# Kernel optimization log

Measured on AMD Instinct MI355X. Metric: run time of the kernel, lower is better.

## Reference

```python
import jax, jax.numpy as jnp
import numpy as np

EPS = 1e-5  # BatchNorm1d default eps
E = 64      # embedding_dim
H = 64      # h_dim


def _mlp(x, W1, b1, gamma, beta, W2, b2):
    # Linear -> BatchNorm1d (training-mode batch stats) -> ReLU -> Linear
    h = x @ W1.T + b1
    mu = h.mean(axis=0)
    var = h.var(axis=0)  # biased variance, as BatchNorm normalization uses
    h = jax.nn.relu((h - mu) * jax.lax.rsqrt(var + EPS) * gamma + beta)
    return h @ W2.T + b2


def _lstm_step(h, c, x, Wih, Whh, bih, bhh):
    # PyTorch LSTM gate order: i, f, g, o
    gates = x @ Wih.T + bih + h @ Whh.T + bhh
    i, f, g, o = jnp.split(gates, 4, axis=-1)
    c = jax.nn.sigmoid(f) * c + jax.nn.sigmoid(i) * jnp.tanh(g)
    h = jax.nn.sigmoid(o) * jnp.tanh(c)
    return h, c


def setup_inputs() -> dict:
    key = jax.random.key(0)
    ks = jax.random.split(key, 16)
    OBS_LEN, BATCH = 8, 131072
    f32 = jnp.float32
    inp = {
        "obs_traj": jax.random.uniform(ks[0], (OBS_LEN, BATCH, 2), dtype=f32) * 100.0,
        # spatial_embedding MLP: [2, 16, 64]
        "se_W1": jax.random.normal(ks[1], (16, 2), f32) * 0.5,
        "se_b1": jnp.zeros((16,), f32),
        "se_gamma": jnp.ones((16,), f32),
        "se_beta": jnp.zeros((16,), f32),
        "se_W2": jax.random.normal(ks[2], (E, 16), f32) * 0.2,
        "se_b2": jnp.zeros((E,), f32),
        # hidden2pos MLP: [64, 16, 2]
        "hp_W1": jax.random.normal(ks[3], (16, H), f32) * 0.1,
        "hp_b1": jnp.zeros((16,), f32),
        "hp_gamma": jnp.ones((16,), f32),
        "hp_beta": jnp.zeros((16,), f32),
        "hp_W2": jax.random.normal(ks[4], (2, 16), f32) * 0.2,
        "hp_b2": jnp.zeros((2,), f32),
        # LSTM(64, 64, num_layers=1)
        "Wih": jax.random.normal(ks[5], (4 * H, E), f32) * 0.1,
        "Whh": jax.random.normal(ks[6], (4 * H, H), f32) * 0.1,
        "bih": jnp.zeros((4 * H,), f32),
        "bhh": jnp.zeros((4 * H,), f32),
        "x_max": 100,
        "y_max": 100,
        "pred_len": 12,
    }
    return inp


def reference(obs_traj, se_W1, se_b1, se_gamma, se_beta, se_W2, se_b2,
              hp_W1, hp_b1, hp_gamma, hp_beta, hp_W2, hp_b2,
              Wih, Whh, bih, bhh, x_max, y_max, pred_len):
    T, B, _ = obs_traj.shape
    xy_max = jnp.asarray([x_max, y_max], dtype=obs_traj.dtype)
    obs = obs_traj / xy_max  # (T, B, 2)

    # embed observed trajectory: (T*B, 2) -> (T, B, E)
    emb = _mlp(obs.reshape(-1, 2), se_W1, se_b1, se_gamma, se_beta, se_W2, se_b2)
    emb = emb.reshape(T, B, E)

    h0 = jnp.zeros((B, H), obs.dtype)
    c0 = jnp.zeros((B, H), obs.dtype)

    def enc(carry, x):
        h, c = carry
        h, c = _lstm_step(h, c, x, Wih, Whh, bih, bhh)
        return (h, c), None

    (h, c), _ = jax.lax.scan(enc, (h0, c0), emb)

    def dec(carry, _):
        h, c, last_pos = carry
        pos_rel = _mlp(h, hp_W1, hp_b1, hp_gamma, hp_beta, hp_W2, hp_b2)  # (B, 2)
        # relative_to_abs over a single step == pos_rel + last_pos
        last_pos = jax.nn.sigmoid(pos_rel + last_pos)
        x = _mlp(last_pos, se_W1, se_b1, se_gamma, se_beta, se_W2, se_b2)  # (B, E)
        h, c = _lstm_step(h, c, x, Wih, Whh, bih, bhh)
        return (h, c, last_pos), last_pos

    _, pred = jax.lax.scan(dec, (h, c, obs[-1]), None, length=pred_len)
    return pred * xy_max  # (pred_len, B, 2)
```

## Files before the change

kernel.cpp:

```cpp
#include <hip/hip_runtime.h>
#include <math.h>


#define TT 8
#define PLEN 12
#define ROWS 64
#define NBUCK 16
#define XSTR 112

typedef unsigned short u16;
typedef short short8 __attribute__((ext_vector_type(8)));
typedef float f4 __attribute__((ext_vector_type(4)));
union U8 { u16 u[8]; short8 v; };

#define ST_ENCM 0
#define ST_HP(d)  (128 + (d)*512)
#define ST_MOM(d) (128 + PLEN*512 + (d)*128)
#define ST_TOTAL  (128 + PLEN*512 + PLEN*128)

struct KP {
  const float *obs;
  const float *seW1,*seb1,*seg,*sebeta,*seW2,*seb2;
  const float *hpW1,*hpb1,*hpg,*hpbeta,*hpW2,*hpb2;
  const float *Wih,*Whh,*bih,*bhh;
  const int *xmax,*ymax;
  float *c,*lastpos,*avalg,*M,*gbias,*gbc;
  u16 *Xg1,*Xg2,*Xg3,*W1G,*W2G,*W3G,*H1G,*H2G,*H3G;
  double *stats;
  float *out;
  int B;
};

__device__ __forceinline__ float finv(float d){
  float r = __builtin_amdgcn_rcpf(d);
  return r*(2.f - d*r);
}
__device__ __forceinline__ float sigf(float x){
  float z = fminf(fmaxf(-x, -80.f), 80.f);
  return finv(1.f + __expf(z));
}
__device__ __forceinline__ float tanhf_(float x){
  float z = fminf(fmaxf(2.f*x, -80.f), 80.f);
  return 1.f - 2.f*finv(__expf(z) + 1.f);
}
__device__ __forceinline__ u16 f2bf(float x){
  union{float f; unsigned u;} v; v.f = x;
  unsigned r = v.u + 0x7FFFu + ((v.u >> 16) & 1u);
  return (u16)(r >> 16);
}
__device__ __forceinline__ float bf2f(u16 b){
  union{unsigned u; float f;} v; v.u = ((unsigned)b) << 16; return v.f;
}
__device__ __forceinline__ void split3(float x, u16& a, u16& b, u16& c){
  a = f2bf(x);
  float r1 = x - bf2f(a);
  b = f2bf(r1);
  float r2 = r1 - bf2f(b);
  c = f2bf(r2);
}

#define MF6(A1c,A2c,A3c,b1,b2,b3,accv) \
  accv = __builtin_amdgcn_mfma_f32_16x16x32_bf16(A1c, b1, accv, 0,0,0); \
  accv = __builtin_amdgcn_mfma_f32_16x16x32_bf16(A1c, b2, accv, 0,0,0); \
  accv = __builtin_amdgcn_mfma_f32_16x16x32_bf16(A2c, b1, accv, 0,0,0); \
  accv = __builtin_amdgcn_mfma_f32_16x16x32_bf16(A2c, b2, accv, 0,0,0); \
  accv = __builtin_amdgcn_mfma_f32_16x16x32_bf16(A1c, b3, accv, 0,0,0); \
  accv = __builtin_amdgcn_mfma_f32_16x16x32_bf16(A3c, b1, accv, 0,0,0);

__device__ __forceinline__ void fold_se_mom(const KP& P, const double* stb, double N,
                                            float* sef, int tid){
  if (tid < 16){
    double Sx=0, Sy=0, Sxx=0, Syy=0, Sxy=0;
    for (int b = 0; b < NBUCK; ++b){
      const double* m = stb + b*8;
      Sx += m[0]; Sy += m[1]; Sxx += m[2]; Syy += m[3]; Sxy += m[4];
    }
    double a = (double)P.seW1[2*tid], bb = (double)P.seW1[2*tid+1], cb = (double)P.seb1[tid];
    double S1 = a*Sx + bb*Sy + N*cb;
    double S2 = a*a*Sxx + bb*bb*Syy + 2.0*a*bb*Sxy + 2.0*a*cb*Sx + 2.0*bb*cb*Sy + N*cb*cb;
    double mu = S1/N, var = S2/N - mu*mu;
    float sc = rsqrtf((float)var + 1e-5f) * P.seg[tid];
    float sh = P.sebeta[tid] - (float)mu*sc;
    sef[tid]      = P.seW1[2*tid]*sc;
    sef[16 + tid] = P.seW1[2*tid+1]*sc;
    sef[32 + tid] = P.seb1[tid]*sc + sh;
  }
}

__device__ __forceinline__ void do_epilogue(f4 (&acc)[2][4], float (&cr)[2][4],
                                            u16* X1, u16* X2, u16* X3,
                                            bool first, int lane, int wid){
  const int c = lane & 15, q = lane >> 4;
  #pragma unroll
  for (int ci = 0; ci < 2; ++ci){
    const int j = (2*wid + ci)*4 + q;
    #pragma unroll
    for (int rt = 0; rt < 4; ++rt){
      const int r = rt*16 + c;
      float iv = acc[ci][rt].x, fv = acc[ci][rt].y;
      float gv = acc[ci][rt].z, ov = acc[ci][rt].w;
      float cp = first ? 0.f : cr[ci][rt];
      float cn = sigf(fv)*cp + sigf(iv)*tanhf_(gv);
      cr[ci][rt] = cn;
      float hn = sigf(ov)*tanhf_(cn);
      u16 a, b, cc2;
      split3(hn, a, b, cc2);
      X1[r*XSTR + j] = a; X2[r*XSTR + j] = b; X3[r*XSTR + j] = cc2;
    }
  }
}

__device__ __forceinline__ void tail_xg_aval(const KP& P, long row0,
                                             const u16* X1, const u16* X2, const u16* X3,
                                             double* redd, double* st,
                                             int tid, int lane, int wid, int blk){
  {
    int r = tid >> 3, ch = tid & 7;
    *(short8*)&P.Xg1[(row0 + r)*64 + ch*8] = *(const short8*)&X1[r*XSTR + ch*8];
    *(short8*)&P.Xg2[(row0 + r)*64 + ch*8] = *(const short8*)&X2[r*XSTR + ch*8];
    *(short8*)&P.Xg3[(row0 + r)*64 + ch*8] = *(const short8*)&X3[r*XSTR + ch*8];
  }
  if (wid < 4){
    const int c = lane & 15, q = lane >> 4, rt = wid;
    f4 av = *(const f4*)&P.hpb1[q*4];
    #pragma unroll
    for (int kc = 0; kc < 2; ++kc){
      const int aoff = (lane & 15)*64 + kc*32 + q*8;
      short8 HA1 = *(const short8*)&P.H1G[aoff];
      short8 HA2 = *(const short8*)&P.H2G[aoff];
      short8 HA3 = *(const short8*)&P.H3G[aoff];
      const int boff = (rt*16 + c)*XSTR + kc*32 + q*8;
      short8 b1 = *(const short8*)&X1[boff];
      short8 b2 = *(const short8*)&X2[boff];
      short8 b3 = *(const short8*)&X3[boff];
      MF6(HA1, HA2, HA3, b1, b2, b3, av);
    }
    #pragma unroll
    for (int i = 0; i < 4; ++i)
      P.avalg[(long)(q*4 + i)*P.B + row0 + rt*16 + c] = av[i];
    #pragma unroll
    for (int i = 0; i < 4; ++i){
      double s = (double)av[i];
      double s2 = s*s;
      #pragma unroll
      for (int off = 8; off; off >>= 1){
        s  += __shfl_down(s,  off, 16);
        s2 += __shfl_down(s2, off, 16);
      }
      if (c == 0){
        redd[wid*32 + q*4 + i]      = s;
        redd[wid*32 + 16 + q*4 + i] = s2;
      }
    }
  }
  __syncthreads();
  if (tid < 32){
    double s = redd[tid] + redd[32 + tid] + redd[64 + tid] + redd[96 + tid];
    atomicAdd(&st[(blk & (NBUCK-1))*32 + tid], s);
  }
}

__global__ __launch_bounds__(256) void k_prep(KP P){
  const int g = threadIdx.x;
  const float* __restrict__ wr = P.Wih + g*64;
  double gb = (double)P.bih[g] + (double)P.bhh[g];
  for (int e = 0; e < 64; ++e) gb += (double)wr[e]*(double)P.seb2[e];
  P.gbias[g] = (float)gb;
  for (int q = 0; q < 16; ++q){
    double m = 0.0;
    for (int e = 0; e < 64; ++e) m += (double)wr[e]*(double)P.seW2[e*16+q];
    P.M[g*16+q] = (float)m;
  }
}

__global__ __launch_bounds__(256) void k_prep2(KP P){
  const int cidx = threadIdx.x;
  const int gate = cidx & 3, j = cidx >> 2;
  P.gbc[cidx] = P.gbias[gate*64 + j];
  for (int k = 0; k < 96; ++k){
    float w = 0.f;
    if (k < 64)      w = P.Whh[(gate*64 + j)*64 + k];
    else if (k < 80) w = P.M[(gate*64 + j)*16 + (k - 64)];
    u16 a, b, c;
    split3(w, a, b, c);
    P.W1G[cidx*96 + k] = a;
    P.W2G[cidx*96 + k] = b;
    P.W3G[cidx*96 + k] = c;
  }
  if (cidx < 16){
    for (int k = 0; k < 64; ++k){
      u16 a, b, c;
      split3(P.hpW1[cidx*64 + k], a, b, c);
      P.H1G[cidx*64 + k] = a;
      P.H2G[cidx*64 + k] = b;
      P.H3G[cidx*64 + k] = c;
    }
  }
}

__global__ __launch_bounds__(512) void k_stats_mom(KP P){
  __shared__ double redd[5*9];
  const int tid = threadIdx.x, lane = tid & 63, wid = tid >> 6;
  const int row = blockIdx.x*512 + tid;
  const int B = P.B;
  const float xm = (float)P.xmax[0], ym = (float)P.ymax[0];
  double sx=0, sy=0, sxx=0, syy=0, sxy=0;
  #pragma unroll 1
  for (int t = 0; t < TT; ++t){
    float2 o = ((const float2*)P.obs)[(long)t*B + row];
    float x = o.x/xm, y = o.y/ym;
    sx += (double)x; sy += (double)y;
    sxx += (double)x*(double)x; syy += (double)y*(double)y;
    sxy += (double)x*(double)y;
  }
  #pragma unroll
  for (int off = 32; off; off >>= 1){
    sx  += __shfl_down(sx,  off, 64);
    sy  += __shfl_down(sy,  off, 64);
    sxx += __shfl_down(sxx, off, 64);
    syy += __shfl_down(syy, off, 64);
    sxy += __shfl_down(sxy, off, 64);
  }
  if (lane == 0){
    redd[0*9+wid]=sx; redd[1*9+wid]=sy; redd[2*9+wid]=sxx;
    redd[3*9+wid]=syy; redd[4*9+wid]=sxy;
  }
  __syncthreads();
  if (tid < 5){
    double s = 0.0;
    for (int w = 0; w < 8; ++w) s += redd[tid*9 + w];
    atomicAdd(&P.stats[ST_ENCM + (blockIdx.x & (NBUCK-1))*8 + tid], s);
  }
}

__global__ __launch_bounds__(512) void k_enc(KP P){
  __shared__ __align__(16) u16 X1[ROWS*XSTR];
  __shared__ __align__(16) u16 X2[ROWS*XSTR];
  __shared__ __align__(16) u16 X3[ROWS*XSTR];
  __shared__ float sef[48];
  __shared__ double redd[128];
  const int tid = threadIdx.x, lane = tid & 63, wid = tid >> 6;
  const int B = P.B;
  const long row0 = (long)blockIdx.x * ROWS;
  const float xm = (float)P.xmax[0], ym = (float)P.ymax[0];

  for (int m = tid; m < 3584; m += 512){
    ((unsigned*)X1)[m] = 0u; ((unsigned*)X2)[m] = 0u; ((unsigned*)X3)[m] = 0u;
  }
  fold_se_mom(P, P.stats + ST_ENCM, 8.0*(double)B, sef, tid);
  __syncthreads();

  if (tid < ROWS){
    float2 o = ((const float2*)P.obs)[row0 + tid];
    float p0 = o.x/xm, p1 = o.y/ym;
    #pragma unroll
    for (int q = 0; q < 16; ++q){
      float tv = sef[q]*p0 + sef[16+q]*p1 + sef[32+q];
      tv = tv > 0.f ? tv : 0.f;
      u16 a, b, c;
      split3(tv, a, b, c);
      X1[tid*XSTR + 64 + q] = a; X2[tid*XSTR + 64 + q] = b; X3[tid*XSTR + 64 + q] = c;
    }
  }
  __syncthreads();

  const int c = lane & 15, q = lane >> 4;
  float cr[2][4];
  f4 acc[2][4];

  #pragma unroll 1
  for (int t = 0; t < TT; ++t){
    #pragma unroll
    for (int ci = 0; ci < 2; ++ci){
      f4 bias = *(const f4*)&P.gbc[(2*wid + ci)*16 + q*4];
      #pragma unroll
      for (int rt = 0; rt < 4; ++rt) acc[ci][rt] = bias;
    }
    #pragma unroll
    for (int rt = 0; rt < 4; ++rt){
      #pragma unroll
      for (int kc = 0; kc < 3; ++kc){
        const int boff = (rt*16 + c)*XSTR + kc*32 + q*8;
        short8 b1 = *(const short8*)&X1[boff];
        short8 b2 = *(const short8*)&X2[boff];
        short8 b3 = *(const short8*)&X3[boff];
        #pragma unroll
        for (int ci = 0; ci < 2; ++ci){
          const int aoff = ((2*wid + ci)*16 + c)*96 + kc*32 + q*8;
          short8 A1 = *(const short8*)&P.W1G[aoff];
          short8 A2 = *(const short8*)&P.W2G[aoff];
          short8 A3 = *(const short8*)&P.W3G[aoff];
          MF6(A1, A2, A3, b1, b2, b3, acc[ci][rt]);
        }
      }
    }
    __syncthreads();
    do_epilogue(acc, cr, X1, X2, X3, t == 0, lane, wid);
    if (t < TT-1 && tid < ROWS){
      float2 o = ((const float2*)P.obs)[(long)(t+1)*B + row0 + tid];
      float p0 = o.x/xm, p1 = o.y/ym;
      #pragma unroll
      for (int qq = 0; qq < 16; ++qq){
        float tv = sef[qq]*p0 + sef[16+qq]*p1 + sef[32+qq];
        tv = tv > 0.f ? tv : 0.f;
        u16 a, b, cc;
        split3(tv, a, b, cc);
        X1[tid*XSTR + 64 + qq] = a; X2[tid*XSTR + 64 + qq] = b; X3[tid*XSTR + 64 + qq] = cc;
      }
    }
    __syncthreads();
  }

  #pragma unroll
  for (int ci = 0; ci < 2; ++ci){
    const int j = (2*wid + ci)*4 + q;
    #pragma unroll
    for (int rt = 0; rt < 4; ++rt)
      P.c[(long)j*B + row0 + rt*16 + c] = cr[ci][rt];
  }
  tail_xg_aval(P, row0, X1, X2, X3, redd, P.stats + ST_HP(0), tid, lane, wid, blockIdx.x);
}

template<bool FIRSTD>
__global__ __launch_bounds__(256) void k_dec_pos(KP P, int d){
  __shared__ float hpf[32];
  __shared__ double redd[5*5];
  const int tid = threadIdx.x, lane = tid & 63, wid = tid >> 6;
  const int B = P.B;
  const int row = blockIdx.x*256 + tid;
  if (tid < 16){
    const double* st = P.stats + ST_HP(d);
    double s = 0.0, s2 = 0.0;
    for (int b = 0; b < NBUCK; ++b){ s += st[b*32 + tid]; s2 += st[b*32 + 16 + tid]; }
    double invN = 1.0/(double)B;
    double mu = s*invN, var = s2*invN - mu*mu;
    float sc = rsqrtf((float)var + 1e-5f) * P.hpg[tid];
    hpf[tid] = sc;
    hpf[16+tid] = P.hpbeta[tid] - (float)mu*sc;
  }
  __syncthreads();

  float r0v = P.hpb2[0], r1v = P.hpb2[1];
  #pragma unroll
  for (int qq = 0; qq < 16; ++qq){
    float a = P.avalg[(long)qq*B + row];
    a = a*hpf[qq] + hpf[16+qq];
    a = a > 0.f ? a : 0.f;
    r0v += a*P.hpW2[qq]; r1v += a*P.hpW2[16+qq];
  }
  const float xm = (float)P.xmax[0], ym = (float)P.ymax[0];
  float l0, l1;
  if constexpr (FIRSTD){
    float2 o = ((const float2*)P.obs)[(long)(TT-1)*B + row];
    l0 = o.x/xm; l1 = o.y/ym;
  } else {
    float2 lp = ((const float2*)P.lastpos)[row];
    l0 = lp.x; l1 = lp.y;
  }
  l0 = sigf(r0v + l0);
  l1 = sigf(r1v + l1);
  ((float2*)P.lastpos)[row] = make_float2(l0, l1);
  ((float2*)P.out)[(long)d*B + row] = make_float2(l0*xm, l1*ym);

  double a0=l0, a1=l1, a2=(double)l0*(double)l0, a3=(double)l1*(double)l1, a4=(double)l0*(double)l1;
  #pragma unroll
  for (int off = 32; off; off >>= 1){
    a0 += __shfl_down(a0, off, 64); a1 += __shfl_down(a1, off, 64);
    a2 += __shfl_down(a2, off, 64); a3 += __shfl_down(a3, off, 64);
    a4 += __shfl_down(a4, off, 64);
  }
  if (lane == 0){
    redd[0*5+wid]=a0; redd[1*5+wid]=a1; redd[2*5+wid]=a2;
    redd[3*5+wid]=a3; redd[4*5+wid]=a4;
  }
  __syncthreads();
  if (tid < 5){
    double s = 0.0;
    for (int w = 0; w < 4; ++w) s += redd[tid*5 + w];
    atomicAdd(&P.stats[ST_MOM(d) + (blockIdx.x & (NBUCK-1))*8 + tid], s);
  }
}

template<int DUMMY>
__global__ __launch_bounds__(512) void k_dec_lstm(KP P, int d){
  __shared__ __align__(16) u16 X1[ROWS*XSTR];
  __shared__ __align__(16) u16 X2[ROWS*XSTR];
  __shared__ __align__(16) u16 X3[ROWS*XSTR];
  __shared__ float sef[48];
  __shared__ double redd[128];
  const int tid = threadIdx.x, lane = tid & 63, wid = tid >> 6;
  const int B = P.B;
  const long row0 = (long)blockIdx.x * ROWS;
  const int c = lane & 15, q = lane >> 4;

  fold_se_mom(P, P.stats + ST_MOM(d), (double)B, sef, tid);
  __syncthreads();

  short8 vb1[4], vb2[4], vb3[4];
  {
    const short8 z = {0,0,0,0,0,0,0,0};
    #pragma unroll
    for (int rt = 0; rt < 4; ++rt){ vb1[rt] = z; vb2[rt] = z; vb3[rt] = z; }
    if (q < 2){
      #pragma unroll
      for (int rt = 0; rt < 4; ++rt){
        float2 lp = ((const float2*)P.lastpos)[row0 + rt*16 + c];
        U8 u1, u2, u3;
        #pragma unroll
        for (int j = 0; j < 8; ++j){
          const int ch = q*8 + j;
          float tv = sef[ch]*lp.x + sef[16+ch]*lp.y + sef[32+ch];
          tv = tv > 0.f ? tv : 0.f;
          split3(tv, u1.u[j], u2.u[j], u3.u[j]);
        }
        vb1[rt] = u1.v; vb2[rt] = u2.v; vb3[rt] = u3.v;
      }
    }
  }
  float cr[2][4];
  #pragma unroll
  for (int ci = 0; ci < 2; ++ci){
    const int j = (2*wid + ci)*4 + q;
    #pragma unroll
    for (int rt = 0; rt < 4; ++rt)
      cr[ci][rt] = P.c[(long)j*B + row0 + rt*16 + c];
  }

  f4 acc[2][4];
  #pragma unroll
  for (int ci = 0; ci < 2; ++ci){
    f4 bias = *(const f4*)&P.gbc[(2*wid + ci)*16 + q*4];
    #pragma unroll
    for (int rt = 0; rt < 4; ++rt) acc[ci][rt] = bias;
  }
  #pragma unroll
  for (int rt = 0; rt < 4; ++rt){
    const long gb = (row0 + rt*16 + c)*64;
    #pragma unroll
    for (int kc = 0; kc < 2; ++kc){
      short8 b1 = *(const short8*)&P.Xg1[gb + kc*32 + q*8];
      short8 b2 = *(const short8*)&P.Xg2[gb + kc*32 + q*8];
      short8 b3 = *(const short8*)&P.Xg3[gb + kc*32 + q*8];
      #pragma unroll
      for (int ci = 0; ci < 2; ++ci){
        const int aoff = ((2*wid + ci)*16 + c)*96 + kc*32 + q*8;
        short8 A1 = *(const short8*)&P.W1G[aoff];
        short8 A2 = *(const short8*)&P.W2G[aoff];
        short8 A3 = *(const short8*)&P.W3G[aoff];
        MF6(A1, A2, A3, b1, b2, b3, acc[ci][rt]);
      }
    }
    #pragma unroll
    for (int ci = 0; ci < 2; ++ci){
      const int aoff = ((2*wid + ci)*16 + c)*96 + 2*32 + q*8;
      short8 A1 = *(const short8*)&P.W1G[aoff];
      short8 A2 = *(const short8*)&P.W2G[aoff];
      short8 A3 = *(const short8*)&P.W3G[aoff];
      MF6(A1, A2, A3, vb1[rt], vb2[rt], vb3[rt], acc[ci][rt]);
    }
  }

  do_epilogue(acc, cr, X1, X2, X3, false, lane, wid);
  #pragma unroll
  for (int ci = 0; ci < 2; ++ci){
    const int j = (2*wid + ci)*4 + q;
    #pragma unroll
    for (int rt = 0; rt < 4; ++rt)
      P.c[(long)j*B + row0 + rt*16 + c] = cr[ci][rt];
  }
  __syncthreads();
  tail_xg_aval(P, row0, X1, X2, X3, redd, P.stats + ST_HP(d+1), tid, lane, wid, blockIdx.x);
}

extern "C" void kernel_launch(void* const* d_in, const int* in_sizes, int n_in,
                              void* d_out, int out_size, void* d_ws, size_t ws_size,
                              hipStream_t stream){
  KP P;
  P.obs    = (const float*)d_in[0];
  P.seW1   = (const float*)d_in[1];
  P.seb1   = (const float*)d_in[2];
  P.seg    = (const float*)d_in[3];
  P.sebeta = (const float*)d_in[4];
  P.seW2   = (const float*)d_in[5];
  P.seb2   = (const float*)d_in[6];
  P.hpW1   = (const float*)d_in[7];
  P.hpb1   = (const float*)d_in[8];
  P.hpg    = (const float*)d_in[9];
  P.hpbeta = (const float*)d_in[10];
  P.hpW2   = (const float*)d_in[11];
  P.hpb2   = (const float*)d_in[12];
  P.Wih    = (const float*)d_in[13];
  P.Whh    = (const float*)d_in[14];
  P.bih    = (const float*)d_in[15];
  P.bhh    = (const float*)d_in[16];
  P.xmax   = (const int*)d_in[17];
  P.ymax   = (const int*)d_in[18];

  const int B = in_sizes[0] / (TT*2);
  P.B = B;
  float* ws = (float*)d_ws;
  P.Xg1     = (u16*)(ws);
  P.Xg2     = (u16*)(ws + (size_t)32*B);
  P.c       = ws + (size_t)64*B;
  P.lastpos = ws + (size_t)128*B;
  P.Xg3     = (u16*)(ws + (size_t)130*B);
  P.avalg   = ws + (size_t)162*B;
  float* tail = ws + (size_t)178*B;
  P.M     = tail;
  P.gbias = tail + 4096;
  P.gbc   = tail + 4352;
  P.W1G   = (u16*)(tail + 4608);
  P.W2G   = (u16*)(tail + 4608 + 12288);
  P.W3G   = (u16*)(tail + 4608 + 24576);
  P.H1G   = (u16*)(tail + 4608 + 36864);
  P.H2G   = (u16*)(tail + 4608 + 37376);
  P.H3G   = (u16*)(tail + 4608 + 37888);
  P.stats = (double*)(tail + 4608 + 38400);
  P.out   = (float*)d_out;

  hipMemsetAsync(P.stats, 0, ST_TOTAL*sizeof(double), stream);

  k_prep     <<<1, 256, 0, stream>>>(P);
  k_prep2    <<<1, 256, 0, stream>>>(P);
  k_stats_mom<<<B/512, 512, 0, stream>>>(P);
  k_enc      <<<B/ROWS, 512, 0, stream>>>(P);

  for (int d = 0; d < PLEN; ++d){
    if (d == 0) k_dec_pos<true ><<<B/256, 256, 0, stream>>>(P, d);
    else        k_dec_pos<false><<<B/256, 256, 0, stream>>>(P, d);
    if (d < PLEN-1) k_dec_lstm<0><<<B/ROWS, 512, 0, stream>>>(P, d);
  }
}
```

Baseline: 1.938 ms.

## Hoist encoder weights into registers, shrink LDS stride, merge prep kernels, widen dec_pos

Several changes at once. The encoder kernel now loads its split-bf16 LSTM weight fragments and bias into registers once, instead of re-reading them from global memory every timestep. The LDS row stride drops from 112 to 104, which cuts shared-memory footprint and changes the bank pattern. The two prep kernels are merged into one launch with a __syncthreads between phases, and k_dec_pos moves to 512-thread blocks. Holding the weights in registers adds register pressure in the encoder, which could reduce occupancy.

Result: faster. 1.851 ms (-4.5%).

```diff
diff --git a/kernel.cpp b/kernel.cpp
--- a/kernel.cpp
+++ b/kernel.cpp
@@ -6,7 +6,7 @@
 #define PLEN 12
 #define ROWS 64
 #define NBUCK 16
-#define XSTR 112
+#define XSTR 104
 
 typedef unsigned short u16;
 typedef short short8 __attribute__((ext_vector_type(8)));
@@ -162,38 +162,39 @@
 
 __global__ __launch_bounds__(256) void k_prep(KP P){
   const int g = threadIdx.x;
-  const float* __restrict__ wr = P.Wih + g*64;
-  double gb = (double)P.bih[g] + (double)P.bhh[g];
-  for (int e = 0; e < 64; ++e) gb += (double)wr[e]*(double)P.seb2[e];
-  P.gbias[g] = (float)gb;
-  for (int q = 0; q < 16; ++q){
-    double m = 0.0;
-    for (int e = 0; e < 64; ++e) m += (double)wr[e]*(double)P.seW2[e*16+q];
-    P.M[g*16+q] = (float)m;
-  }
-}
-
-__global__ __launch_bounds__(256) void k_prep2(KP P){
-  const int cidx = threadIdx.x;
-  const int gate = cidx & 3, j = cidx >> 2;
-  P.gbc[cidx] = P.gbias[gate*64 + j];
-  for (int k = 0; k < 96; ++k){
-    float w = 0.f;
-    if (k < 64)      w = P.Whh[(gate*64 + j)*64 + k];
-    else if (k < 80) w = P.M[(gate*64 + j)*16 + (k - 64)];
-    u16 a, b, c;
-    split3(w, a, b, c);
-    P.W1G[cidx*96 + k] = a;
-    P.W2G[cidx*96 + k] = b;
-    P.W3G[cidx*96 + k] = c;
-  }
-  if (cidx < 16){
-    for (int k = 0; k < 64; ++k){
+  {
+    const float* __restrict__ wr = P.Wih + g*64;
+    double gb = (double)P.bih[g] + (double)P.bhh[g];
+    for (int e = 0; e < 64; ++e) gb += (double)wr[e]*(double)P.seb2[e];
+    P.gbias[g] = (float)gb;
+    for (int q = 0; q < 16; ++q){
+      double m = 0.0;
+      for (int e = 0; e < 64; ++e) m += (double)wr[e]*(double)P.seW2[e*16+q];
+      P.M[g*16+q] = (float)m;
+    }
+  }
+  __syncthreads();
+  {
+    const int cidx = g, gate = cidx & 3, j = cidx >> 2;
+    P.gbc[cidx] = P.gbias[gate*64 + j];
+    for (int k = 0; k < 96; ++k){
+      float w = 0.f;
+      if (k < 64)      w = P.Whh[(gate*64 + j)*64 + k];
+      else if (k < 80) w = P.M[(gate*64 + j)*16 + (k - 64)];
       u16 a, b, c;
-      split3(P.hpW1[cidx*64 + k], a, b, c);
-      P.H1G[cidx*64 + k] = a;
-      P.H2G[cidx*64 + k] = b;
-      P.H3G[cidx*64 + k] = c;
+      split3(w, a, b, c);
+      P.W1G[cidx*96 + k] = a;
+      P.W2G[cidx*96 + k] = b;
+      P.W3G[cidx*96 + k] = c;
+    }
+    if (cidx < 16){
+      for (int k = 0; k < 64; ++k){
+        u16 a, b, c;
+        split3(P.hpW1[cidx*64 + k], a, b, c);
+        P.H1G[cidx*64 + k] = a;
+        P.H2G[cidx*64 + k] = b;
+        P.H3G[cidx*64 + k] = c;
+      }
     }
   }
 }
@@ -243,8 +244,24 @@
   const int B = P.B;
   const long row0 = (long)blockIdx.x * ROWS;
   const float xm = (float)P.xmax[0], ym = (float)P.ymax[0];
-
-  for (int m = tid; m < 3584; m += 512){
+  const int c = lane & 15, q = lane >> 4;
+
+  short8 A1r[2][3], A2r[2][3], A3r[2][3];
+  f4 biasr[2];
+  #pragma unroll
+  for (int ci = 0; ci < 2; ++ci){
+    const int crow = (2*wid + ci)*16 + c;
+    #pragma unroll
+    for (int kc = 0; kc < 3; ++kc){
+      const int aoff = crow*96 + kc*32 + q*8;
+      A1r[ci][kc] = *(const short8*)&P.W1G[aoff];
+      A2r[ci][kc] = *(const short8*)&P.W2G[aoff];
+      A3r[ci][kc] = *(const short8*)&P.W3G[aoff];
+    }
+    biasr[ci] = *(const f4*)&P.gbc[(2*wid + ci)*16 + q*4];
+  }
+
+  for (int m = tid; m < (ROWS*XSTR)/2; m += 512){
     ((unsigned*)X1)[m] = 0u; ((unsigned*)X2)[m] = 0u; ((unsigned*)X3)[m] = 0u;
   }
   fold_se_mom(P, P.stats + ST_ENCM, 8.0*(double)B, sef, tid);
@@ -254,28 +271,25 @@
     float2 o = ((const float2*)P.obs)[row0 + tid];
     float p0 = o.x/xm, p1 = o.y/ym;
     #pragma unroll
-    for (int q = 0; q < 16; ++q){
-      float tv = sef[q]*p0 + sef[16+q]*p1 + sef[32+q];
+    for (int qq = 0; qq < 16; ++qq){
+      float tv = sef[qq]*p0 + sef[16+qq]*p1 + sef[32+qq];
       tv = tv > 0.f ? tv : 0.f;
-      u16 a, b, c;
-      split3(tv, a, b, c);
-      X1[tid*XSTR + 64 + q] = a; X2[tid*XSTR + 64 + q] = b; X3[tid*XSTR + 64 + q] = c;
-    }
-  }
-  __syncthreads();
-
-  const int c = lane & 15, q = lane >> 4;
+      u16 a, b, cc;
+      split3(tv, a, b, cc);
+      X1[tid*XSTR + 64 + qq] = a; X2[tid*XSTR + 64 + qq] = b; X3[tid*XSTR + 64 + qq] = cc;
+    }
+  }
+  __syncthreads();
+
   float cr[2][4];
   f4 acc[2][4];
 
   #pragma unroll 1
   for (int t = 0; t < TT; ++t){
     #pragma unroll
-    for (int ci = 0; ci < 2; ++ci){
-      f4 bias = *(const f4*)&P.gbc[(2*wid + ci)*16 + q*4];
+    for (int ci = 0; ci < 2; ++ci)
       #pragma unroll
-      for (int rt = 0; rt < 4; ++rt) acc[ci][rt] = bias;
-    }
+      for (int rt = 0; rt < 4; ++rt) acc[ci][rt] = biasr[ci];
     #pragma unroll
     for (int rt = 0; rt < 4; ++rt){
       #pragma unroll
@@ -286,11 +300,7 @@
         short8 b3 = *(const short8*)&X3[boff];
         #pragma unroll
         for (int ci = 0; ci < 2; ++ci){
-          const int aoff = ((2*wid + ci)*16 + c)*96 + kc*32 + q*8;
-          short8 A1 = *(const short8*)&P.W1G[aoff];
-          short8 A2 = *(const short8*)&P.W2G[aoff];
-          short8 A3 = *(const short8*)&P.W3G[aoff];
-          MF6(A1, A2, A3, b1, b2, b3, acc[ci][rt]);
+          MF6(A1r[ci][kc], A2r[ci][kc], A3r[ci][kc], b1, b2, b3, acc[ci][rt]);
         }
       }
     }
@@ -322,12 +332,12 @@
 }
 
 template<bool FIRSTD>
-__global__ __launch_bounds__(256) void k_dec_pos(KP P, int d){
+__global__ __launch_bounds__(512) void k_dec_pos(KP P, int d){
   __shared__ float hpf[32];
-  __shared__ double redd[5*5];
+  __shared__ double redd[5*9];
   const int tid = threadIdx.x, lane = tid & 63, wid = tid >> 6;
   const int B = P.B;
-  const int row = blockIdx.x*256 + tid;
+  const int row = blockIdx.x*512 + tid;
   if (tid < 16){
     const double* st = P.stats + ST_HP(d);
     double s = 0.0, s2 = 0.0;
@@ -370,13 +380,13 @@
     a4 += __shfl_down(a4, off, 64);
   }
   if (lane == 0){
-    redd[0*5+wid]=a0; redd[1*5+wid]=a1; redd[2*5+wid]=a2;
-    redd[3*5+wid]=a3; redd[4*5+wid]=a4;
+    redd[0*9+wid]=a0; redd[1*9+wid]=a1; redd[2*9+wid]=a2;
+    redd[3*9+wid]=a3; redd[4*9+wid]=a4;
   }
   __syncthreads();
   if (tid < 5){
     double s = 0.0;
-    for (int w = 0; w < 4; ++w) s += redd[tid*5 + w];
+    for (int w = 0; w < 8; ++w) s += redd[tid*9 + w];
     atomicAdd(&P.stats[ST_MOM(d) + (blockIdx.x & (NBUCK-1))*8 + tid], s);
   }
 }
@@ -521,13 +531,12 @@
   hipMemsetAsync(P.stats, 0, ST_TOTAL*sizeof(double), stream);
 
   k_prep     <<<1, 256, 0, stream>>>(P);
-  k_prep2    <<<1, 256, 0, stream>>>(P);
   k_stats_mom<<<B/512, 512, 0, stream>>>(P);
   k_enc      <<<B/ROWS, 512, 0, stream>>>(P);
 
   for (int d = 0; d < PLEN; ++d){
-    if (d == 0) k_dec_pos<true ><<<B/256, 256, 0, stream>>>(P, d);
-    else        k_dec_pos<false><<<B/256, 256, 0, stream>>>(P, d);
+    if (d == 0) k_dec_pos<true ><<<B/512, 512, 0, stream>>>(P, d);
+    else        k_dec_pos<false><<<B/512, 512, 0, stream>>>(P, d);
     if (d < PLEN-1) k_dec_lstm<0><<<B/ROWS, 512, 0, stream>>>(P, d);
   }
 }
```
